# Performance work log

Measured on AMD Instinct MI355X. Metric: run time of the kernel, lower is better.

The kernel has to match this reference:

```python
import jax, jax.numpy as jnp
import numpy as np

Q, C, T, D_IN, D_H = 512, 512, 128, 512, 256


def setup_inputs() -> dict:
    key = jax.random.key(0)
    ks = jax.random.split(key, 8)
    s_in = 1.0 / np.sqrt(D_IN)
    s_h = 1.0 / np.sqrt(D_H)
    return {
        "audio": jax.random.normal(ks[0], (Q, T, D_IN), jnp.float32),
        "video": jax.random.normal(ks[1], (C, T, D_IN), jnp.float32),
        "a_w1": jax.random.normal(ks[2], (D_IN, D_H), jnp.float32) * s_in,
        "a_b1": jnp.zeros((D_H,), jnp.float32),
        "a_w2": jax.random.normal(ks[3], (D_H, D_H), jnp.float32) * s_h,
        "a_b2": jnp.zeros((D_H,), jnp.float32),
        "v_w1": jax.random.normal(ks[4], (D_IN, D_H), jnp.float32) * s_in,
        "v_b1": jnp.zeros((D_H,), jnp.float32),
        "v_w2": jax.random.normal(ks[5], (D_H, D_H), jnp.float32) * s_h,
        "v_b2": jnp.zeros((D_H,), jnp.float32),
        "W": jax.random.normal(ks[6], (D_H, D_H), jnp.float32) * s_h,
        "max_lag": 4,
    }


def _mlp(x, w1, b1, w2, b2):
    # Linear -> ReLU -> Linear
    h = jnp.maximum(x @ w1 + b1, 0.0)
    return h @ w2 + b2


def reference(audio, video, a_w1, a_b1, a_w2, a_b2,
              v_w1, v_b1, v_w2, v_b2, W, max_lag):
    a = _mlp(audio, a_w1, a_b1, a_w2, a_b2)   # [Q, T, D_H]
    v = _mlp(video, v_w1, v_b1, v_w2, v_b2)   # [C, T, D_H]
    # roll along time commutes with the per-frame linear map, so project once
    pv = jnp.einsum('ctd,df->ctf', v, W)      # [C, T, D_H]
    best = None
    for delta in range(-max_lag, max_lag + 1):
        shifted = jnp.roll(pv, delta, axis=1)
        score = jnp.einsum('qtd,ctd->qc', a, shifted)  # [Q, C]
        best = score if best is None else jnp.maximum(best, score)
    return best
```

## Files before the change

kernel.cpp:

```cpp
#include <hip/hip_runtime.h>
#include <cstdint>
#include <cstddef>

typedef __attribute__((ext_vector_type(8))) short frag8;
typedef __attribute__((ext_vector_type(4))) float f32x4;

static __device__ __forceinline__ unsigned short f2bf(float f) {
    unsigned int u = __float_as_uint(f);
    u += 0x7fffu + ((u >> 16) & 1u);
    return (unsigned short)(u >> 16);
}

static __device__ __forceinline__ void gll16(const void* g, void* l) {
    __builtin_amdgcn_global_load_lds(
        (const __attribute__((address_space(1))) unsigned int*)g,
        (__attribute__((address_space(3))) unsigned int*)l, 16, 0, 0);
}

template<int AMODE, bool RELU, bool BIAS, bool OUT_BF16, bool CORR>
__global__ __launch_bounds__(256, 3)
void gemm_bt2(const void* __restrict__ Av, const unsigned short* __restrict__ Bt,
              const float* __restrict__ bias, void* __restrict__ Cv,
              int ldA, int ldB, int ldC, int kLen, int Kmask, int Mfull)
{
    __shared__ unsigned short As[(AMODE == 0) ? 128 * 40 : 128 * 32];
    __shared__ unsigned short Bs[128 * 32];

    const int t    = threadIdx.x;
    const int wave = t >> 6;
    const int lane = t & 63;
    const int quad = lane >> 4;
    const int l15  = lane & 15;
    const int wm   = (wave >> 1) * 64;
    const int wn   = (wave & 1) * 64;
    const int m0   = blockIdx.y * 128;
    const int n0   = blockIdx.x * 128;

    int kStart = 0, koff = 0;
    if (CORR) {
        const int z = blockIdx.z;
        kStart = (z & 3) * kLen;
        const int delta = (z >> 2) - 4;
        koff = ((Kmask + 1) - 256 * delta) & Kmask;
    }

    const int rowL = (wave << 5) + (lane >> 2);
    const int qL   = (lane & 3) ^ ((lane >> 3) & 3);
    const size_t offB0 = (size_t)(n0 + rowL) * ldB + qL * 8;
    const size_t offB1 = offB0 + (size_t)16 * ldB;
    const size_t offA0 = (size_t)(m0 + rowL) * ldA + qL * 8;
    const size_t offA1 = offA0 + (size_t)16 * ldA;
    const int swz = quad ^ ((l15 >> 1) & 3);

    f32x4 acc[4][4];
    #pragma unroll
    for (int i = 0; i < 4; ++i)
        #pragma unroll
        for (int j = 0; j < 4; ++j)
            acc[i][j] = (f32x4){0.f, 0.f, 0.f, 0.f};

    for (int k0 = 0; k0 < kLen; k0 += 32) {
        const int kB = (k0 + kStart + koff) & Kmask;
        gll16(Bt + offB0 + kB, &Bs[wave * 1024]);
        gll16(Bt + offB1 + kB, &Bs[wave * 1024 + 512]);
        if (AMODE == 1) {
            const unsigned short* A = (const unsigned short*)Av;
            const int kA = kStart + k0;
            gll16(A + offA0 + kA, &As[wave * 1024]);
            gll16(A + offA1 + kA, &As[wave * 1024 + 512]);
        } else {
            const float* A = (const float*)Av;
            #pragma unroll
            for (int p = 0; p < 4; ++p) {
                int idx = p * 256 + t;
                int row = idx >> 3;
                int col = (idx & 7) * 4;
                const float4 v = *(const float4*)(A + (size_t)(m0 + row) * ldA + (k0 + col));
                unsigned int u0 = (unsigned int)f2bf(v.x) | ((unsigned int)f2bf(v.y) << 16);
                unsigned int u1 = (unsigned int)f2bf(v.z) | ((unsigned int)f2bf(v.w) << 16);
                uint2 pk; pk.x = u0; pk.y = u1;
                *(uint2*)&As[row * 40 + col] = pk;
            }
        }
        __syncthreads();

        frag8 af[4], bf[4];
        #pragma unroll
        for (int i = 0; i < 4; ++i) {
            const int row = wm + i * 16 + l15;
            if (AMODE == 0)
                af[i] = *(const frag8*)&As[row * 40 + quad * 8];
            else
                af[i] = *(const frag8*)&As[(row * 4 + swz) * 8];
        }
        #pragma unroll
        for (int j = 0; j < 4; ++j) {
            const int row = wn + j * 16 + l15;
            bf[j] = *(const frag8*)&Bs[(row * 4 + swz) * 8];
        }
        #pragma unroll
        for (int i = 0; i < 4; ++i)
            #pragma unroll
            for (int j = 0; j < 4; ++j)
                acc[i][j] = __builtin_amdgcn_mfma_f32_16x16x32_bf16(af[i], bf[j], acc[i][j], 0, 0, 0);
        __syncthreads();
    }

    if (CORR) {
        float* C = (float*)Cv + (size_t)blockIdx.z * (size_t)Mfull * (size_t)ldC;
        #pragma unroll
        for (int i = 0; i < 4; ++i) {
            int rg = m0 + wm + i * 16 + quad * 4;
            #pragma unroll
            for (int j = 0; j < 4; ++j) {
                int cg = n0 + wn + j * 16 + l15;
                #pragma unroll
                for (int r = 0; r < 4; ++r)
                    C[(size_t)(rg + r) * ldC + cg] = acc[i][j][r];
            }
        }
    } else {
        #pragma unroll
        for (int i = 0; i < 4; ++i) {
            int rg = m0 + wm + i * 16 + quad * 4;
            #pragma unroll
            for (int j = 0; j < 4; ++j) {
                int cg = n0 + wn + j * 16 + l15;
                float bv = BIAS ? bias[cg] : 0.0f;
                #pragma unroll
                for (int r = 0; r < 4; ++r) {
                    float val = acc[i][j][r] + bv;
                    if (RELU) val = fmaxf(val, 0.0f);
                    if (OUT_BF16)
                        ((unsigned short*)Cv)[(size_t)(rg + r) * ldC + cg] = f2bf(val);
                    else
                        ((float*)Cv)[(size_t)(rg + r) * ldC + cg] = val;
                }
            }
        }
    }
}

__global__ void transp_bf16(const float* __restrict__ src, unsigned short* __restrict__ dst,
                            int R, int C) {
    __shared__ float tile[32][33];
    const int bx = blockIdx.x * 32;
    const int by = blockIdx.y * 32;
    const int tx = threadIdx.x & 31;
    const int ty = threadIdx.x >> 5;
    #pragma unroll
    for (int r = ty; r < 32; r += 8)
        tile[r][tx] = src[(size_t)(by + r) * C + bx + tx];
    __syncthreads();
    #pragma unroll
    for (int c = ty; c < 32; c += 8)
        dst[(size_t)(bx + c) * R + by + tx] = f2bf(tile[tx][c]);
}

__global__ void build_wc(const float* __restrict__ w2, const float* __restrict__ W,
                         const float* __restrict__ b2,
                         unsigned short* __restrict__ WcT, float* __restrict__ bc) {
    __shared__ float wcol[256];
    const int n = blockIdx.x, k = threadIdx.x;
    wcol[k] = W[(size_t)k * 256 + n];
    __syncthreads();
    float s = 0.f;
    #pragma unroll 8
    for (int d = 0; d < 256; ++d) s += w2[(size_t)k * 256 + d] * wcol[d];
    WcT[(size_t)n * 256 + k] = f2bf(s);
    if (k == 0) {
        float tt = 0.f;
        for (int d = 0; d < 256; ++d) tt += b2[d] * wcol[d];
        bc[n] = tt;
    }
}

__global__ void reduce_max9(const float* __restrict__ partial, float* __restrict__ out) {
    const int idx = blockIdx.x * blockDim.x + threadIdx.x;
    float best = -3.4e38f;
    #pragma unroll
    for (int dz = 0; dz < 9; ++dz) {
        float s = 0.f;
        #pragma unroll
        for (int ks = 0; ks < 4; ++ks)
            s += partial[((size_t)(dz * 4 + ks) << 18) + idx];
        best = fmaxf(best, s);
    }
    out[idx] = best;
}

extern "C" void kernel_launch(void* const* d_in, const int* in_sizes, int n_in,
                              void* d_out, int out_size, void* d_ws, size_t ws_size,
                              hipStream_t stream) {
    const float* audio = (const float*)d_in[0];
    const float* video = (const float*)d_in[1];
    const float* a_w1  = (const float*)d_in[2];
    const float* a_b1  = (const float*)d_in[3];
    const float* a_w2  = (const float*)d_in[4];
    const float* a_b2  = (const float*)d_in[5];
    const float* v_w1  = (const float*)d_in[6];
    const float* v_b1  = (const float*)d_in[7];
    const float* v_w2  = (const float*)d_in[8];
    const float* v_b2  = (const float*)d_in[9];
    const float* Wm    = (const float*)d_in[10];

    char* ws = (char*)d_ws;
    unsigned short* aw1T = (unsigned short*)(ws + 0);
    unsigned short* aw2T = (unsigned short*)(ws + 262144);
    unsigned short* vw1T = (unsigned short*)(ws + 393216);
    unsigned short* WcT  = (unsigned short*)(ws + 655360);
    float*          bc   = (float*)(ws + 786432);
    unsigned short* a_bf = (unsigned short*)(ws + 1048576);
    unsigned short* pv   = (unsigned short*)(ws + 34603008);
    unsigned short* hbuf = (unsigned short*)(ws + 68157440);
    float* partial       = (float*)(ws + 68157440);
    float* out = (float*)d_out;

    transp_bf16<<<dim3(8, 16), 256, 0, stream>>>(a_w1, aw1T, 512, 256);
    transp_bf16<<<dim3(8, 8),  256, 0, stream>>>(a_w2, aw2T, 256, 256);
    transp_bf16<<<dim3(8, 16), 256, 0, stream>>>(v_w1, vw1T, 512, 256);
    build_wc<<<dim3(256), 256, 0, stream>>>(v_w2, Wm, v_b2, WcT, bc);

    gemm_bt2<0, true,  true,  true, false><<<dim3(2, 512), 256, 0, stream>>>(
        audio, aw1T, a_b1, hbuf, 512, 512, 256, 512, 511, 0);
    gemm_bt2<1, false, true,  true, false><<<dim3(2, 512), 256, 0, stream>>>(
        hbuf, aw2T, a_b2, a_bf, 256, 256, 256, 256, 255, 0);

    gemm_bt2<0, true,  true,  true, false><<<dim3(2, 512), 256, 0, stream>>>(
        video, vw1T, v_b1, hbuf, 512, 512, 256, 512, 511, 0);
    gemm_bt2<1, false, true,  true, false><<<dim3(2, 512), 256, 0, stream>>>(
        hbuf, WcT, bc, pv, 256, 256, 256, 256, 255, 0);

    gemm_bt2<1, false, false, false, true><<<dim3(4, 4, 36), 256, 0, stream>>>(
        a_bf, pv, nullptr, partial, 32768, 32768, 512, 8192, 32767, 512);

    reduce_max9<<<dim3(1024), 256, 0, stream>>>(partial, out);
}
```

Before: 586.0 us.

## Batch audio/video MLP GEMMs, stage epilogue through LDS, widen corr K-tile

Merges the four weight-prep kernels into one launch and batches the audio and video MLP GEMMs into single launches over a z-dimension. The MLP epilogue now stages bf16 results in shared memory so global stores are coalesced 16-byte writes. The correlation GEMM becomes its own kernel with a 64-wide K tile and an XOR swizzle, halving the number of loop iterations and barriers. These changes cut launch overhead and improve store and loop efficiency, at the cost of more shared memory per block and lower occupancy (launch bounds 2 instead of 3).

Result: faster. 543.5 us (-7.2%).

```diff
diff --git a/kernel.cpp b/kernel.cpp
--- a/kernel.cpp
+++ b/kernel.cpp
@@ -17,14 +17,25 @@
         (__attribute__((address_space(3))) unsigned int*)l, 16, 0, 0);
 }
 
-template<int AMODE, bool RELU, bool BIAS, bool OUT_BF16, bool CORR>
-__global__ __launch_bounds__(256, 3)
-void gemm_bt2(const void* __restrict__ Av, const unsigned short* __restrict__ Bt,
-              const float* __restrict__ bias, void* __restrict__ Cv,
-              int ldA, int ldB, int ldC, int kLen, int Kmask, int Mfull)
+#define CST 136
+
+template<int AMODE, bool RELU>
+__global__ __launch_bounds__(256, 2)
+void gemm_mlp(const void* __restrict__ A0, const void* __restrict__ A1,
+              const unsigned short* __restrict__ B0, const unsigned short* __restrict__ B1,
+              const float* __restrict__ bias0, const float* __restrict__ bias1,
+              unsigned short* __restrict__ C0, unsigned short* __restrict__ C1,
+              int ldA, int kLen)
 {
-    __shared__ unsigned short As[(AMODE == 0) ? 128 * 40 : 128 * 32];
-    __shared__ unsigned short Bs[128 * 32];
+    __shared__ __align__(16) char smem[CST * 128 * 2];
+    unsigned short* As = (unsigned short*)smem;
+    unsigned short* Bs = (unsigned short*)(smem + (AMODE == 0 ? 10240 : 8192));
+    unsigned short* Cst = (unsigned short*)smem;
+
+    const void* Av = blockIdx.z ? A1 : A0;
+    const unsigned short* Bt = blockIdx.z ? B1 : B0;
+    const float* bias = blockIdx.z ? bias1 : bias0;
+    unsigned short* Cv = blockIdx.z ? C1 : C0;
 
     const int t    = threadIdx.x;
     const int wave = t >> 6;
@@ -36,20 +47,10 @@
     const int m0   = blockIdx.y * 128;
     const int n0   = blockIdx.x * 128;
 
-    int kStart = 0, koff = 0;
-    if (CORR) {
-        const int z = blockIdx.z;
-        kStart = (z & 3) * kLen;
-        const int delta = (z >> 2) - 4;
-        koff = ((Kmask + 1) - 256 * delta) & Kmask;
-    }
-
     const int rowL = (wave << 5) + (lane >> 2);
     const int qL   = (lane & 3) ^ ((lane >> 3) & 3);
-    const size_t offB0 = (size_t)(n0 + rowL) * ldB + qL * 8;
-    const size_t offB1 = offB0 + (size_t)16 * ldB;
+    const size_t offB0 = (size_t)(n0 + rowL) * kLen + qL * 8;
     const size_t offA0 = (size_t)(m0 + rowL) * ldA + qL * 8;
-    const size_t offA1 = offA0 + (size_t)16 * ldA;
     const int swz = quad ^ ((l15 >> 1) & 3);
 
     f32x4 acc[4][4];
@@ -60,14 +61,12 @@
             acc[i][j] = (f32x4){0.f, 0.f, 0.f, 0.f};
 
     for (int k0 = 0; k0 < kLen; k0 += 32) {
-        const int kB = (k0 + kStart + koff) & Kmask;
-        gll16(Bt + offB0 + kB, &Bs[wave * 1024]);
-        gll16(Bt + offB1 + kB, &Bs[wave * 1024 + 512]);
+        gll16(Bt + offB0 + k0, &Bs[wave * 1024]);
+        gll16(Bt + offB0 + (size_t)16 * kLen + k0, &Bs[wave * 1024 + 512]);
         if (AMODE == 1) {
             const unsigned short* A = (const unsigned short*)Av;
-            const int kA = kStart + k0;
-            gll16(A + offA0 + kA, &As[wave * 1024]);
-            gll16(A + offA1 + kA, &As[wave * 1024 + 512]);
+            gll16(A + offA0 + k0, &As[wave * 1024]);
+            gll16(A + offA0 + (size_t)16 * ldA + k0, &As[wave * 1024 + 512]);
         } else {
             const float* A = (const float*)Av;
             #pragma unroll
@@ -106,72 +105,156 @@
         __syncthreads();
     }
 
-    if (CORR) {
-        float* C = (float*)Cv + (size_t)blockIdx.z * (size_t)Mfull * (size_t)ldC;
+    #pragma unroll
+    for (int i = 0; i < 4; ++i) {
+        const int rl = wm + i * 16 + quad * 4;
+        #pragma unroll
+        for (int j = 0; j < 4; ++j) {
+            const int cl = wn + j * 16 + l15;
+            const float bv = bias[n0 + cl];
+            #pragma unroll
+            for (int r = 0; r < 4; ++r) {
+                float val = acc[i][j][r] + bv;
+                if (RELU) val = fmaxf(val, 0.0f);
+                Cst[(rl + r) * CST + cl] = f2bf(val);
+            }
+        }
+    }
+    __syncthreads();
+    #pragma unroll
+    for (int u = 0; u < 8; ++u) {
+        const int c   = u * 256 + t;
+        const int row = c >> 4;
+        const int c8  = (c & 15) * 8;
+        uint4 v = *(const uint4*)&Cst[row * CST + c8];
+        *(uint4*)&Cv[(size_t)(m0 + row) * 256 + n0 + c8] = v;
+    }
+}
+
+__global__ __launch_bounds__(256, 2)
+void gemm_corr(const unsigned short* __restrict__ A, const unsigned short* __restrict__ B,
+               float* __restrict__ partial)
+{
+    __shared__ __align__(16) unsigned short As[128 * 64];
+    __shared__ __align__(16) unsigned short Bs[128 * 64];
+
+    const int t    = threadIdx.x;
+    const int wave = t >> 6;
+    const int lane = t & 63;
+    const int quad = lane >> 4;
+    const int l15  = lane & 15;
+    const int wm   = (wave >> 1) * 64;
+    const int wn   = (wave & 1) * 64;
+    const int m0   = blockIdx.y * 128;
+    const int n0   = blockIdx.x * 128;
+
+    const int z      = blockIdx.z;
+    const int kStart = (z & 3) * 8192;
+    const int delta  = (z >> 2) - 4;
+    const int koff   = (32768 - 256 * delta) & 32767;
+
+    const int rowL = (wave << 5) + (lane >> 3);
+    const int qL   = (lane & 7) ^ ((lane >> 3) & 7);
+    const size_t aBase = (size_t)(m0 + rowL) * 32768 + qL * 8;
+    const size_t bBase = (size_t)(n0 + rowL) * 32768 + qL * 8;
+    unsigned short* AsW = As + wave * 2048;
+    unsigned short* BsW = Bs + wave * 2048;
+    const int swz = l15 & 7;
+
+    f32x4 acc[4][4];
+    #pragma unroll
+    for (int i = 0; i < 4; ++i)
+        #pragma unroll
+        for (int j = 0; j < 4; ++j)
+            acc[i][j] = (f32x4){0.f, 0.f, 0.f, 0.f};
+
+    for (int k0 = 0; k0 < 8192; k0 += 64) {
+        const int kA = kStart + k0;
+        const int kB = (kA + koff) & 32767;
+        #pragma unroll
+        for (int p = 0; p < 4; ++p) {
+            gll16(A + aBase + (size_t)(p * 8) * 32768 + kA, AsW + p * 512);
+            gll16(B + bBase + (size_t)(p * 8) * 32768 + kB, BsW + p * 512);
+        }
+        __syncthreads();
+
+        frag8 af[2][4], bf[2][4];
         #pragma unroll
         for (int i = 0; i < 4; ++i) {
-            int rg = m0 + wm + i * 16 + quad * 4;
-            #pragma unroll
-            for (int j = 0; j < 4; ++j) {
-                int cg = n0 + wn + j * 16 + l15;
+            const int row = wm + i * 16 + l15;
+            #pragma unroll
+            for (int kh = 0; kh < 2; ++kh)
+                af[kh][i] = *(const frag8*)&As[row * 64 + (((kh * 4 + quad) ^ swz) * 8)];
+        }
+        #pragma unroll
+        for (int j = 0; j < 4; ++j) {
+            const int row = wn + j * 16 + l15;
+            #pragma unroll
+            for (int kh = 0; kh < 2; ++kh)
+                bf[kh][j] = *(const frag8*)&Bs[row * 64 + (((kh * 4 + quad) ^ swz) * 8)];
+        }
+        #pragma unroll
+        for (int kh = 0; kh < 2; ++kh)
+            #pragma unroll
+            for (int i = 0; i < 4; ++i)
                 #pragma unroll
-                for (int r = 0; r < 4; ++r)
-                    C[(size_t)(rg + r) * ldC + cg] = acc[i][j][r];
-            }
-        }
+                for (int j = 0; j < 4; ++j)
+                    acc[i][j] = __builtin_amdgcn_mfma_f32_16x16x32_bf16(af[kh][i], bf[kh][j], acc[i][j], 0, 0, 0);
+        __syncthreads();
+    }
+
+    float* C = partial + (size_t)z * 262144;
+    #pragma unroll
+    for (int i = 0; i < 4; ++i) {
+        const int rg = m0 + wm + i * 16 + quad * 4;
+        #pragma unroll
+        for (int j = 0; j < 4; ++j) {
+            const int cg = n0 + wn + j * 16 + l15;
+            #pragma unroll
+            for (int r = 0; r < 4; ++r)
+                C[(size_t)(rg + r) * 512 + cg] = acc[i][j][r];
+        }
+    }
+}
+
+__global__ void prep(const float* __restrict__ a_w1, const float* __restrict__ v_w1,
+                     const float* __restrict__ a_w2, const float* __restrict__ v_w2,
+                     const float* __restrict__ W, const float* __restrict__ v_b2,
+                     unsigned short* __restrict__ aw1T, unsigned short* __restrict__ vw1T,
+                     unsigned short* __restrict__ aw2T,
+                     unsigned short* __restrict__ WcT, float* __restrict__ bc)
+{
+    const int b = blockIdx.x;
+    __shared__ float tl[32][33];
+    __shared__ float wcol[256];
+    if (b < 320) {
+        const float* src; unsigned short* dst; int R, C, tile;
+        if (b < 128)      { src = a_w1; dst = aw1T; R = 512; C = 256; tile = b; }
+        else if (b < 256) { src = v_w1; dst = vw1T; R = 512; C = 256; tile = b - 128; }
+        else              { src = a_w2; dst = aw2T; R = 256; C = 256; tile = b - 256; }
+        const int tilesX = C / 32;
+        const int bx = (tile % tilesX) * 32, by = (tile / tilesX) * 32;
+        const int tx = threadIdx.x & 31, ty = threadIdx.x >> 5;
+        #pragma unroll
+        for (int r = ty; r < 32; r += 8)
+            tl[r][tx] = src[(size_t)(by + r) * C + bx + tx];
+        __syncthreads();
+        #pragma unroll
+        for (int c = ty; c < 32; c += 8)
+            dst[(size_t)(bx + c) * R + by + tx] = f2bf(tl[tx][c]);
     } else {
-        #pragma unroll
-        for (int i = 0; i < 4; ++i) {
-            int rg = m0 + wm + i * 16 + quad * 4;
-            #pragma unroll
-            for (int j = 0; j < 4; ++j) {
-                int cg = n0 + wn + j * 16 + l15;
-                float bv = BIAS ? bias[cg] : 0.0f;
-                #pragma unroll
-                for (int r = 0; r < 4; ++r) {
-                    float val = acc[i][j][r] + bv;
-                    if (RELU) val = fmaxf(val, 0.0f);
-                    if (OUT_BF16)
-                        ((unsigned short*)Cv)[(size_t)(rg + r) * ldC + cg] = f2bf(val);
-                    else
-                        ((float*)Cv)[(size_t)(rg + r) * ldC + cg] = val;
-                }
-            }
-        }
-    }
-}
-
-__global__ void transp_bf16(const float* __restrict__ src, unsigned short* __restrict__ dst,
-                            int R, int C) {
-    __shared__ float tile[32][33];
-    const int bx = blockIdx.x * 32;
-    const int by = blockIdx.y * 32;
-    const int tx = threadIdx.x & 31;
-    const int ty = threadIdx.x >> 5;
-    #pragma unroll
-    for (int r = ty; r < 32; r += 8)
-        tile[r][tx] = src[(size_t)(by + r) * C + bx + tx];
-    __syncthreads();
-    #pragma unroll
-    for (int c = ty; c < 32; c += 8)
-        dst[(size_t)(bx + c) * R + by + tx] = f2bf(tile[tx][c]);
-}
-
-__global__ void build_wc(const float* __restrict__ w2, const float* __restrict__ W,
-                         const float* __restrict__ b2,
-                         unsigned short* __restrict__ WcT, float* __restrict__ bc) {
-    __shared__ float wcol[256];
-    const int n = blockIdx.x, k = threadIdx.x;
-    wcol[k] = W[(size_t)k * 256 + n];
-    __syncthreads();
-    float s = 0.f;
-    #pragma unroll 8
-    for (int d = 0; d < 256; ++d) s += w2[(size_t)k * 256 + d] * wcol[d];
-    WcT[(size_t)n * 256 + k] = f2bf(s);
-    if (k == 0) {
-        float tt = 0.f;
-        for (int d = 0; d < 256; ++d) tt += b2[d] * wcol[d];
-        bc[n] = tt;
+        const int n = b - 320, k = threadIdx.x;
+        wcol[k] = W[(size_t)k * 256 + n];
+        __syncthreads();
+        float s = 0.f;
+        #pragma unroll 8
+        for (int d = 0; d < 256; ++d) s += v_w2[(size_t)k * 256 + d] * wcol[d];
+        WcT[(size_t)n * 256 + k] = f2bf(s);
+        if (k == 0) {
+            float tt = 0.f;
+            for (int d = 0; d < 256; ++d) tt += v_b2[d] * wcol[d];
+            bc[n] = tt;
+        }
     }
 }
 
@@ -206,33 +289,23 @@
 
     char* ws = (char*)d_ws;
     unsigned short* aw1T = (unsigned short*)(ws + 0);
-    unsigned short* aw2T = (unsigned short*)(ws + 262144);
-    unsigned short* vw1T = (unsigned short*)(ws + 393216);
+    unsigned short* vw1T = (unsigned short*)(ws + 262144);
+    unsigned short* aw2T = (unsigned short*)(ws + 524288);
     unsigned short* WcT  = (unsigned short*)(ws + 655360);
     float*          bc   = (float*)(ws + 786432);
     unsigned short* a_bf = (unsigned short*)(ws + 1048576);
     unsigned short* pv   = (unsigned short*)(ws + 34603008);
-    unsigned short* hbuf = (unsigned short*)(ws + 68157440);
+    unsigned short* h_a  = (unsigned short*)(ws + 68157440);
+    unsigned short* h_v  = (unsigned short*)(ws + 101711872);
     float* partial       = (float*)(ws + 68157440);
     float* out = (float*)d_out;
 
-    transp_bf16<<<dim3(8, 16), 256, 0, stream>>>(a_w1, aw1T, 512, 256);
-    transp_bf16<<<dim3(8, 8),  256, 0, stream>>>(a_w2, aw2T, 256, 256);
-    transp_bf16<<<dim3(8, 16), 256, 0, stream>>>(v_w1, vw1T, 512, 256);
-    build_wc<<<dim3(256), 256, 0, stream>>>(v_w2, Wm, v_b2, WcT, bc);
-
-    gemm_bt2<0, true,  true,  true, false><<<dim3(2, 512), 256, 0, stream>>>(
-        audio, aw1T, a_b1, hbuf, 512, 512, 256, 512, 511, 0);
-    gemm_bt2<1, false, true,  true, false><<<dim3(2, 512), 256, 0, stream>>>(
-        hbuf, aw2T, a_b2, a_bf, 256, 256, 256, 256, 255, 0);
-
-    gemm_bt2<0, true,  true,  true, false><<<dim3(2, 512), 256, 0, stream>>>(
-        video, vw1T, v_b1, hbuf, 512, 512, 256, 512, 511, 0);
-    gemm_bt2<1, false, true,  true, false><<<dim3(2, 512), 256, 0, stream>>>(
-        hbuf, WcT, bc, pv, 256, 256, 256, 256, 255, 0);
-
-    gemm_bt2<1, false, false, false, true><<<dim3(4, 4, 36), 256, 0, stream>>>(
-        a_bf, pv, nullptr, partial, 32768, 32768, 512, 8192, 32767, 512);
-
+    prep<<<dim3(576), 256, 0, stream>>>(a_w1, v_w1, a_w2, v_w2, Wm, v_b2,
+                                        aw1T, vw1T, aw2T, WcT, bc);
+    gemm_mlp<0, true><<<dim3(2, 512, 2), 256, 0, stream>>>(
+        audio, video, aw1T, vw1T, a_b1, v_b1, h_a, h_v, 512, 512);
+    gemm_mlp<1, false><<<dim3(2, 512, 2), 256, 0, stream>>>(
+        h_a, h_v, aw2T, WcT, a_b2, bc, a_bf, pv, 256, 256);
+    gemm_corr<<<dim3(4, 4, 36), 256, 0, stream>>>(a_bf, pv, partial);
     reduce_max9<<<dim3(1024), 256, 0, stream>>>(partial, out);
 }
```
